# Kernel tuning notes

Hardware: AMD Instinct MI355X
Metric: run time of the kernel (lower is better)

## Reference

```python
import jax, jax.numpy as jnp
import numpy as np

K = 1024  # num_embeddings
D = 256   # embedding_dim
COMMIT = 0.25

def setup_inputs() -> dict:
    key = jax.random.key(0)
    k1, k2 = jax.random.split(key)
    z = jax.random.normal(k1, (32, 256, 32, 32), dtype=jnp.float32)
    # matches nn.Embedding init uniform_(-1/K, 1/K)
    emb = jax.random.uniform(k2, (K, D), dtype=jnp.float32, minval=-1.0 / K, maxval=1.0 / K)
    return {"z": z, "emb": emb}

def reference(z, emb):
    B, C, H, W = z.shape
    zp = jnp.transpose(z, (0, 2, 3, 1))            # (B,H,W,C)
    z_flat = zp.reshape(-1, C)                      # (N,D)
    # squared euclidean distances (N,K)
    d = (jnp.sum(z_flat * z_flat, axis=1, keepdims=True)
         + jnp.sum(emb * emb, axis=1)
         - 2.0 * z_flat @ emb.T)
    idx = jnp.argmin(d, axis=1)                     # (N,)
    quantized_flat = emb[idx]                       # gather == one-hot @ emb
    quantized = quantized_flat.reshape(zp.shape)    # (B,H,W,C)
    e_latent_loss = jnp.mean((jax.lax.stop_gradient(quantized) - zp) ** 2)
    q_latent_loss = jnp.mean((quantized - jax.lax.stop_gradient(zp)) ** 2)
    loss = q_latent_loss + COMMIT * e_latent_loss
    # straight-through estimator
    quantized_st = zp + jax.lax.stop_gradient(quantized - zp)
    # perplexity: avg one-hot probs == normalized counts
    N = z_flat.shape[0]
    counts = jnp.zeros((K,), dtype=jnp.float32).at[idx].add(1.0)
    avg_probs = counts / N
    perplexity = jnp.exp(-jnp.sum(avg_probs * jnp.log(avg_probs + 1e-10)))
    out = jnp.transpose(quantized_st, (0, 3, 1, 2))  # (B,C,H,W)
    return (out, loss, perplexity)
```

## Files before the change

### kernel.cpp

```cpp
#include <hip/hip_runtime.h>
#include <math.h>

#define KC 1024
#define DD 256
#define NROWS 32768
#define NELEM 8388608

typedef _Float16 f16;
typedef __attribute__((ext_vector_type(8))) _Float16 f16x8;
typedef __attribute__((ext_vector_type(16))) float f32x16;

#define KEY_SCALE 2097152.0f
#define KEY_INV   (1.0f / 2097152.0f)

__global__ void vq_prep_kernel(const float* __restrict__ emb, f16* __restrict__ emb_h,
                               float* __restrict__ c_sq, unsigned* __restrict__ stat_done) {
    const int tid = threadIdx.x;
    const int gt = blockIdx.x * 256 + tid;
    if (gt == 0) *stat_done = 0u;
    {
        int k = blockIdx.x * 4 + (tid >> 6);
        int lane = tid & 63;
        float4 v = *(const float4*)(emb + (size_t)k * DD + lane * 4);
        float s = v.x * v.x + v.y * v.y + v.z * v.z + v.w * v.w;
        #pragma unroll
        for (int off = 32; off > 0; off >>= 1) s += __shfl_down(s, off);
        if (lane == 0) c_sq[k] = s;
    }
    if (gt < 32768) {
        int code = gt & 1023;
        int kg = gt >> 10;
        const float* p = emb + (size_t)code * DD + kg * 8;
        float4 v0 = *(const float4*)p;
        float4 v1 = *(const float4*)(p + 4);
        f16x8 hcv;
        hcv[0] = (f16)v0.x; hcv[1] = (f16)v0.y; hcv[2] = (f16)v0.z; hcv[3] = (f16)v0.w;
        hcv[4] = (f16)v1.x; hcv[5] = (f16)v1.y; hcv[6] = (f16)v1.z; hcv[7] = (f16)v1.w;
        *(f16x8*)(emb_h + (size_t)gt * 8) = hcv;
    }
}

__global__ __launch_bounds__(512, 4)
void vq_argmin_kernel(const float* __restrict__ z, const f16* __restrict__ emb_h,
                      const float* __restrict__ c_sq, int* __restrict__ idx_g,
                      float* __restrict__ loss_blk) {
    __shared__ __align__(16) f16 z_s[32 * 128 * 8];
    __shared__ int   bl_key[8][128];
    __shared__ float zsq_part[8][128];
    __shared__ float lsum2[2];

    const int tid = threadIdx.x;
    const int n0 = blockIdx.x * 128;
    const int b = n0 >> 10;
    const int hw0 = n0 & 1023;

    {
        const int r2 = tid & 63;
        const int kq = tid >> 6;
        #pragma unroll
        for (int rh = 0; rh < 2; ++rh) {
            const int r = rh * 64 + r2;
            const float* zp = z + (size_t)b * (DD * 1024) + hw0 + r;
            float sq = 0.f;
            #pragma unroll
            for (int it = 0; it < 4; ++it) {
                int kg = kq * 4 + it;
                f16x8 hv;
                #pragma unroll
                for (int j = 0; j < 8; ++j) {
                    float v = zp[(size_t)(kg * 8 + j) * 1024];
                    sq += v * v;
                    hv[j] = (f16)v;
                }
                *(f16x8*)&z_s[(kg * 128 + r) * 8] = hv;
            }
            zsq_part[kq][r] = sq;
        }
    }
    __syncthreads();

    const int m = tid & 31;
    const int h = (tid >> 5) & 1;
    const int w = tid >> 6;

    int kmin0 = 0x7FFFFFFF;
    int kmin1 = 0x7FFFFFFF;
    int kmin2 = 0x7FFFFFFF;
    int kmin3 = 0x7FFFFFFF;

    for (int c = 0; c < 4; ++c) {
        const int cb = w * 128 + c * 32;
        const f16* ebp = emb_h + (size_t)h * 8192 + (size_t)(cb + m) * 8;

        f32x16 acc0, acc1, acc2, acc3;
        #pragma unroll
        for (int i = 0; i < 16; ++i) {
            acc0[i] = 0.f; acc1[i] = 0.f; acc2[i] = 0.f; acc3[i] = 0.f;
        }

        #pragma unroll 2
        for (int ks = 0; ks < 16; ++ks) {
            const f16* za = z_s + ((size_t)(2 * ks + h) * 128 + m) * 8;
            f16x8 zb0 = *(const f16x8*)(za);
            f16x8 zb1 = *(const f16x8*)(za + 256);
            f16x8 zb2 = *(const f16x8*)(za + 512);
            f16x8 zb3 = *(const f16x8*)(za + 768);
            f16x8 ea  = *(const f16x8*)(ebp + (size_t)ks * 16384);
            acc0 = __builtin_amdgcn_mfma_f32_32x32x16_f16(ea, zb0, acc0, 0, 0, 0);
            acc1 = __builtin_amdgcn_mfma_f32_32x32x16_f16(ea, zb1, acc1, 0, 0, 0);
            acc2 = __builtin_amdgcn_mfma_f32_32x32x16_f16(ea, zb2, acc2, 0, 0, 0);
            acc3 = __builtin_amdgcn_mfma_f32_32x32x16_f16(ea, zb3, acc3, 0, 0, 0);
        }

        #pragma unroll
        for (int reg = 0; reg < 16; ++reg) {
            int code = cb + (reg & 3) + 8 * (reg >> 2) + 4 * h;
            float cs = c_sq[code];
            float s0 = fmaf(-2.f, acc0[reg], cs);
            float s1 = fmaf(-2.f, acc1[reg], cs);
            float s2 = fmaf(-2.f, acc2[reg], cs);
            float s3 = fmaf(-2.f, acc3[reg], cs);
            kmin0 = min(kmin0, (int)(s0 * KEY_SCALE) * 1024 + code);
            kmin1 = min(kmin1, (int)(s1 * KEY_SCALE) * 1024 + code);
            kmin2 = min(kmin2, (int)(s2 * KEY_SCALE) * 1024 + code);
            kmin3 = min(kmin3, (int)(s3 * KEY_SCALE) * 1024 + code);
        }
    }

    kmin0 = min(kmin0, __shfl_xor(kmin0, 32));
    kmin1 = min(kmin1, __shfl_xor(kmin1, 32));
    kmin2 = min(kmin2, __shfl_xor(kmin2, 32));
    kmin3 = min(kmin3, __shfl_xor(kmin3, 32));
    if (h == 0) {
        bl_key[w][m]      = kmin0;
        bl_key[w][32 + m] = kmin1;
        bl_key[w][64 + m] = kmin2;
        bl_key[w][96 + m] = kmin3;
    }
    __syncthreads();

    if (tid < 128) {
        int k = bl_key[0][tid];
        #pragma unroll
        for (int w2 = 1; w2 < 8; ++w2) k = min(k, bl_key[w2][tid]);
        idx_g[n0 + tid] = k & 1023;
        float zq = 0.f;
        #pragma unroll
        for (int p = 0; p < 8; ++p) zq += zsq_part[p][tid];
        float lr = (float)(k >> 10) * KEY_INV + zq;
        #pragma unroll
        for (int off = 32; off > 0; off >>= 1) lr += __shfl_down(lr, off);
        if ((tid & 63) == 0) lsum2[tid >> 6] = lr;
    }
    __syncthreads();
    if (tid == 0) loss_blk[blockIdx.x] = lsum2[0] + lsum2[1];
}

__global__ __launch_bounds__(512, 4)
void vq_out_kernel(const float* __restrict__ emb, const int* __restrict__ idx_g,
                   const float* __restrict__ loss_blk, int* __restrict__ hist_g,
                   unsigned* __restrict__ stat_done, float* __restrict__ out,
                   float* __restrict__ out_tail) {
    __shared__ float Qt[128][65];
    __shared__ int   idx_s[64];
    __shared__ int   hist[KC];
    __shared__ float wsum[8];
    __shared__ int   flag_s;

    const int tid = threadIdx.x;
    const int bid = blockIdx.x;

    if (bid >= 1024) {
        const int j = bid - 1024;
        for (int k = tid; k < KC; k += 512) hist[k] = 0;
        __syncthreads();
        #pragma unroll
        for (int it = 0; it < 8; ++it)
            atomicAdd(&hist[idx_g[j * 4096 + it * 512 + tid]], 1);
        __syncthreads();
        for (int k = tid; k < KC; k += 512) hist_g[j * KC + k] = hist[k];
        __threadfence();
        if (tid == 0) flag_s = (atomicAdd(stat_done, 1u) == 7u) ? 1 : 0;
        __syncthreads();
        if (!flag_s) return;
        __threadfence();

        float s = 0.f;
        for (int k = tid; k < KC; k += 512) {
            int c = 0;
            #pragma unroll
            for (int p = 0; p < 8; ++p) c += atomicAdd(&hist_g[p * KC + k], 0);
            float pr = (float)c * (1.0f / (float)NROWS);
            s += pr * logf(pr + 1e-10f);
        }
        float lv = (tid < 256) ? loss_blk[tid] : 0.f;
        #pragma unroll
        for (int off = 32; off > 0; off >>= 1) {
            s  += __shfl_down(s, off);
            lv += __shfl_down(lv, off);
        }
        if ((tid & 63) == 0) { wsum[tid >> 6] = s; Qt[0][tid >> 6] = lv; }
        __syncthreads();
        if (tid == 0) {
            float ent = 0.f, loss_tot = 0.f;
            #pragma unroll
            for (int p = 0; p < 8; ++p) { ent += wsum[p]; loss_tot += Qt[0][p]; }
            out_tail[0] = 1.25f * loss_tot * (1.0f / (float)NELEM);
            out_tail[1] = expf(-ent);
        }
        return;
    }

    const int tile = bid >> 1;
    const int ch0 = (bid & 1) * 128;
    const int n0 = tile * 64;
    const int b = n0 >> 10;
    const int hw0 = n0 & 1023;

    if (tid < 64) idx_s[tid] = idx_g[n0 + tid];
    __syncthreads();

    {
        int r = tid & 63;
        int p = tid >> 6;
        const float* ep = emb + (size_t)idx_s[r] * DD + ch0 + p * 16;
        float4 v0 = *(const float4*)(ep);
        float4 v1 = *(const float4*)(ep + 4);
        float4 v2 = *(const float4*)(ep + 8);
        float4 v3 = *(const float4*)(ep + 12);
        float vv[16] = {v0.x, v0.y, v0.z, v0.w, v1.x, v1.y, v1.z, v1.w,
                        v2.x, v2.y, v2.z, v2.w, v3.x, v3.y, v3.z, v3.w};
        #pragma unroll
        for (int g = 0; g < 16; ++g)
            Qt[p * 16 + g][r] = vv[g];
    }
    __syncthreads();

    {
        int lane = tid & 63;
        int w = tid >> 6;
        const size_t base = (size_t)b * (DD * 1024) + hw0 + lane;
        #pragma unroll
        for (int g = 0; g < 16; ++g) {
            int ch = w * 16 + g;
            out[base + (size_t)(ch0 + ch) * 1024] = Qt[ch][lane];
        }
    }
}

extern "C" void kernel_launch(void* const* d_in, const int* in_sizes, int n_in,
                              void* d_out, int out_size, void* d_ws, size_t ws_size,
                              hipStream_t stream) {
    const float* z = (const float*)d_in[0];
    const float* emb = (const float*)d_in[1];
    float* out = (float*)d_out;

    char* wsb = (char*)d_ws;
    f16* emb_h = (f16*)wsb;
    float* c_sq = (float*)(wsb + 524288);
    int* idx_g = (int*)(wsb + 528384);
    float* loss_blk = (float*)(wsb + 659456);
    int* hist_g = (int*)(wsb + 661504);
    unsigned* stat_done = (unsigned*)(wsb + 694272);

    hipLaunchKernelGGL(vq_prep_kernel, dim3(256), dim3(256), 0, stream,
                       emb, emb_h, c_sq, stat_done);
    hipLaunchKernelGGL(vq_argmin_kernel, dim3(256), dim3(512), 0, stream,
                       z, emb_h, c_sq, idx_g, loss_blk);
    hipLaunchKernelGGL(vq_out_kernel, dim3(1032), dim3(512), 0, stream,
                       emb, idx_g, loss_blk, hist_g, stat_done, out, out + NELEM);
}
```

Measured before the change: 117.9 us.

## Fuse quantized-output gather/transpose into argmin kernel, split stats into small kernel

The gather of selected codebook rows and the transposed NCHW write move into the argmin kernel's epilogue. Each block writes its own 128 rows in four passes, reusing the z staging shared memory as the transpose buffer. This drops the idx_g round trip for the output path and the large separate output launch, and the histogram/perplexity work moves to an 8-block kernel. The trade-off is that the output writes now run on only 256 blocks, which may give less memory-level parallelism than the previous 1024 output blocks.

```diff
diff --git a/kernel.cpp b/kernel.cpp
--- a/kernel.cpp
+++ b/kernel.cpp
@@ -41,13 +41,18 @@
 }
 
 __global__ __launch_bounds__(512, 4)
-void vq_argmin_kernel(const float* __restrict__ z, const f16* __restrict__ emb_h,
-                      const float* __restrict__ c_sq, int* __restrict__ idx_g,
-                      float* __restrict__ loss_blk) {
-    __shared__ __align__(16) f16 z_s[32 * 128 * 8];
+void vq_main_kernel(const float* __restrict__ z, const float* __restrict__ emb,
+                    const f16* __restrict__ emb_h, const float* __restrict__ c_sq,
+                    int* __restrict__ idx_g, float* __restrict__ loss_blk,
+                    float* __restrict__ out) {
+    __shared__ __align__(16) char smem[65536];
     __shared__ int   bl_key[8][128];
     __shared__ float zsq_part[8][128];
+    __shared__ int   idx_s[128];
     __shared__ float lsum2[2];
+
+    f16* z_s = (f16*)smem;
+    float (*Qt)[65] = (float(*)[65])smem;
 
     const int tid = threadIdx.x;
     const int n0 = blockIdx.x * 128;
@@ -143,7 +148,9 @@
         int k = bl_key[0][tid];
         #pragma unroll
         for (int w2 = 1; w2 < 8; ++w2) k = min(k, bl_key[w2][tid]);
-        idx_g[n0 + tid] = k & 1023;
+        int i = k & 1023;
+        idx_s[tid] = i;
+        idx_g[n0 + tid] = i;
         float zq = 0.f;
         #pragma unroll
         for (int p = 0; p < 8; ++p) zq += zsq_part[p][tid];
@@ -154,97 +161,86 @@
     }
     __syncthreads();
     if (tid == 0) loss_blk[blockIdx.x] = lsum2[0] + lsum2[1];
+
+    #pragma unroll
+    for (int q = 0; q < 4; ++q) {
+        const int rh = q >> 1;
+        const int ch0 = (q & 1) * 128;
+        {
+            int r = tid & 63;
+            int p = tid >> 6;
+            const float* ep = emb + (size_t)idx_s[rh * 64 + r] * DD + ch0 + p * 16;
+            float4 v0 = *(const float4*)(ep);
+            float4 v1 = *(const float4*)(ep + 4);
+            float4 v2 = *(const float4*)(ep + 8);
+            float4 v3 = *(const float4*)(ep + 12);
+            float vv[16] = {v0.x, v0.y, v0.z, v0.w, v1.x, v1.y, v1.z, v1.w,
+                            v2.x, v2.y, v2.z, v2.w, v3.x, v3.y, v3.z, v3.w};
+            #pragma unroll
+            for (int g = 0; g < 16; ++g)
+                Qt[p * 16 + g][r] = vv[g];
+        }
+        __syncthreads();
+        {
+            int lane = tid & 63;
+            const size_t base = (size_t)b * (DD * 1024) + hw0 + rh * 64 + lane;
+            #pragma unroll
+            for (int g = 0; g < 16; ++g) {
+                int ch = w * 16 + g;
+                out[base + (size_t)(ch0 + ch) * 1024] = Qt[ch][lane];
+            }
+        }
+        __syncthreads();
+    }
 }
 
 __global__ __launch_bounds__(512, 4)
-void vq_out_kernel(const float* __restrict__ emb, const int* __restrict__ idx_g,
-                   const float* __restrict__ loss_blk, int* __restrict__ hist_g,
-                   unsigned* __restrict__ stat_done, float* __restrict__ out,
-                   float* __restrict__ out_tail) {
-    __shared__ float Qt[128][65];
-    __shared__ int   idx_s[64];
+void vq_stat_kernel(const int* __restrict__ idx_g, const float* __restrict__ loss_blk,
+                    int* __restrict__ hist_g, unsigned* __restrict__ stat_done,
+                    float* __restrict__ out_tail) {
     __shared__ int   hist[KC];
     __shared__ float wsum[8];
+    __shared__ float lsumw[8];
     __shared__ int   flag_s;
 
     const int tid = threadIdx.x;
-    const int bid = blockIdx.x;
-
-    if (bid >= 1024) {
-        const int j = bid - 1024;
-        for (int k = tid; k < KC; k += 512) hist[k] = 0;
-        __syncthreads();
-        #pragma unroll
-        for (int it = 0; it < 8; ++it)
-            atomicAdd(&hist[idx_g[j * 4096 + it * 512 + tid]], 1);
-        __syncthreads();
-        for (int k = tid; k < KC; k += 512) hist_g[j * KC + k] = hist[k];
-        __threadfence();
-        if (tid == 0) flag_s = (atomicAdd(stat_done, 1u) == 7u) ? 1 : 0;
-        __syncthreads();
-        if (!flag_s) return;
-        __threadfence();
-
-        float s = 0.f;
-        for (int k = tid; k < KC; k += 512) {
-            int c = 0;
-            #pragma unroll
-            for (int p = 0; p < 8; ++p) c += atomicAdd(&hist_g[p * KC + k], 0);
-            float pr = (float)c * (1.0f / (float)NROWS);
-            s += pr * logf(pr + 1e-10f);
-        }
-        float lv = (tid < 256) ? loss_blk[tid] : 0.f;
-        #pragma unroll
-        for (int off = 32; off > 0; off >>= 1) {
-            s  += __shfl_down(s, off);
-            lv += __shfl_down(lv, off);
-        }
-        if ((tid & 63) == 0) { wsum[tid >> 6] = s; Qt[0][tid >> 6] = lv; }
-        __syncthreads();
-        if (tid == 0) {
-            float ent = 0.f, loss_tot = 0.f;
-            #pragma unroll
-            for (int p = 0; p < 8; ++p) { ent += wsum[p]; loss_tot += Qt[0][p]; }
-            out_tail[0] = 1.25f * loss_tot * (1.0f / (float)NELEM);
-            out_tail[1] = expf(-ent);
-        }
-        return;
-    }
-
-    const int tile = bid >> 1;
-    const int ch0 = (bid & 1) * 128;
-    const int n0 = tile * 64;
-    const int b = n0 >> 10;
-    const int hw0 = n0 & 1023;
-
-    if (tid < 64) idx_s[tid] = idx_g[n0 + tid];
-    __syncthreads();
-
-    {
-        int r = tid & 63;
-        int p = tid >> 6;
-        const float* ep = emb + (size_t)idx_s[r] * DD + ch0 + p * 16;
-        float4 v0 = *(const float4*)(ep);
-        float4 v1 = *(const float4*)(ep + 4);
-        float4 v2 = *(const float4*)(ep + 8);
-        float4 v3 = *(const float4*)(ep + 12);
-        float vv[16] = {v0.x, v0.y, v0.z, v0.w, v1.x, v1.y, v1.z, v1.w,
-                        v2.x, v2.y, v2.z, v2.w, v3.x, v3.y, v3.z, v3.w};
-        #pragma unroll
-        for (int g = 0; g < 16; ++g)
-            Qt[p * 16 + g][r] = vv[g];
-    }
-    __syncthreads();
-
-    {
-        int lane = tid & 63;
-        int w = tid >> 6;
-        const size_t base = (size_t)b * (DD * 1024) + hw0 + lane;
-        #pragma unroll
-        for (int g = 0; g < 16; ++g) {
-            int ch = w * 16 + g;
-            out[base + (size_t)(ch0 + ch) * 1024] = Qt[ch][lane];
-        }
+    const int j = blockIdx.x;
+
+    for (int k = tid; k < KC; k += 512) hist[k] = 0;
+    __syncthreads();
+    #pragma unroll
+    for (int it = 0; it < 8; ++it)
+        atomicAdd(&hist[idx_g[j * 4096 + it * 512 + tid]], 1);
+    __syncthreads();
+    for (int k = tid; k < KC; k += 512) hist_g[j * KC + k] = hist[k];
+    __threadfence();
+    if (tid == 0) flag_s = (atomicAdd(stat_done, 1u) == 7u) ? 1 : 0;
+    __syncthreads();
+    if (!flag_s) return;
+    __threadfence();
+
+    float s = 0.f;
+    for (int k = tid; k < KC; k += 512) {
+        int c = 0;
+        #pragma unroll
+        for (int p = 0; p < 8; ++p) c += atomicAdd(&hist_g[p * KC + k], 0);
+        float pr = (float)c * (1.0f / (float)NROWS);
+        s += pr * logf(pr + 1e-10f);
+    }
+    float lv = (tid < 256) ? loss_blk[tid] : 0.f;
+    #pragma unroll
+    for (int off = 32; off > 0; off >>= 1) {
+        s  += __shfl_down(s, off);
+        lv += __shfl_down(lv, off);
+    }
+    if ((tid & 63) == 0) { wsum[tid >> 6] = s; lsumw[tid >> 6] = lv; }
+    __syncthreads();
+    if (tid == 0) {
+        float ent = 0.f, loss_tot = 0.f;
+        #pragma unroll
+        for (int p = 0; p < 8; ++p) { ent += wsum[p]; loss_tot += lsumw[p]; }
+        out_tail[0] = 1.25f * loss_tot * (1.0f / (float)NELEM);
+        out_tail[1] = expf(-ent);
     }
 }
 
@@ -265,8 +261,8 @@
 
     hipLaunchKernelGGL(vq_prep_kernel, dim3(256), dim3(256), 0, stream,
                        emb, emb_h, c_sq, stat_done);
-    hipLaunchKernelGGL(vq_argmin_kernel, dim3(256), dim3(512), 0, stream,
-                       z, emb_h, c_sq, idx_g, loss_blk);
-    hipLaunchKernelGGL(vq_out_kernel, dim3(1032), dim3(512), 0, stream,
-                       emb, idx_g, loss_blk, hist_g, stat_done, out, out + NELEM);
-}
+    hipLaunchKernelGGL(vq_main_kernel, dim3(256), dim3(512), 0, stream,
+                       z, emb, emb_h, c_sq, idx_g, loss_blk, out);
+    hipLaunchKernelGGL(vq_stat_kernel, dim3(8), dim3(512), 0, stream,
+                       idx_g, loss_blk, hist_g, stat_done, out + NELEM);
+}
```

New measurement: 118.9 us. About the same (+0.8%).
